# Optimization experiments

Measured on AMD Instinct MI355X. Metric: run time of the kernel, lower is better.

Reference implementation:

```python
import jax, jax.numpy as jnp
import numpy as np

MAX_DIST = 10
N_OUT = 8


def setup_inputs() -> dict:
    key = jax.random.key(0)
    k1, k2 = jax.random.split(key)
    B, N = 32, 512
    adjacency = jax.random.uniform(k1, (B, N, N), dtype=jnp.float32)
    node_mask = jnp.ones((B, N), dtype=bool)
    # learned embedding table: (max_distance + 2, n_out)
    emb = jax.random.normal(k2, (MAX_DIST + 2, N_OUT), dtype=jnp.float32)
    return {"adjacency": adjacency, "node_mask": node_mask, "emb": emb}


def reference(adjacency, node_mask, emb):
    # BFS distances computed under no_grad in the original -> stop_gradient
    adjacency = jax.lax.stop_gradient(adjacency)
    B, N, _ = adjacency.shape
    adj_bin = adjacency > 0.5
    adj_sym = adj_bin | jnp.swapaxes(adj_bin, -1, -2)
    pair_valid = node_mask[:, :, None] & node_mask[:, None, :]  # (B,N,N)
    adj_sym = adj_sym & pair_valid
    adj_f = adj_sym.astype(jnp.float32)

    UNREACH = MAX_DIST + 1
    eye = jnp.eye(N, dtype=bool)[None]                 # (1,N,N)
    dist = jnp.where(eye, 0, UNREACH).astype(jnp.int32)  # broadcasts to (B,N,N) later
    reach = jnp.broadcast_to(eye, (B, N, N))

    # iterative BFS: reach_{k+1} = (reach_k @ adj > 0) | reach_k
    for k in range(1, MAX_DIST + 1):
        reach_next = (jnp.einsum('bij,bjk->bik', reach.astype(jnp.float32), adj_f) > 0) | reach
        frontier = reach_next & ~reach
        dist = jnp.where(frontier, jnp.int32(k), dist)
        reach = reach_next

    dist = jnp.where(pair_valid, dist, UNREACH)  # invalid pairs -> UNREACHABLE
    return emb[dist]  # (B,N,N,n_out)
```

## Files before the change

### kernel.cpp

```cpp
#include <hip/hip_runtime.h>
#include <stdint.h>

typedef unsigned long long u64;
typedef float vf4 __attribute__((ext_vector_type(4)));

#define NB 32
#define N 512
#define MAXD 10
#define NW 8
#define ST 516
#define PB 8

__global__ __launch_bounds__(256) void k1_pack(const float* __restrict__ adj,
                                               const int* __restrict__ mask,
                                               u64* __restrict__ gsym) {
    __shared__ float ldsA[64 * 65];
    __shared__ float ldsB[64 * 65];
    __shared__ unsigned char mI[64], mJ[64];
    int p = blockIdx.x;
    int b = blockIdx.y;
    int ti = 0;
    while (p >= 8 - ti) { p -= 8 - ti; ++ti; }
    int tj = ti + p;
    int i0 = ti * 64, j0 = tj * 64;
    int t = threadIdx.x;
    if (t < 64) mI[t] = (mask[b * N + i0 + t] != 0);
    else if (t < 128) mJ[t - 64] = (mask[b * N + j0 + (t - 64)] != 0);
    const float* Ab = adj + (size_t)b * N * N;
    #pragma unroll
    for (int s = 0; s < 4; ++s) {
        int idx = t + 256 * s;
        int r = idx >> 4, c4 = idx & 15;
        float4 va = *(const float4*)&Ab[(size_t)(i0 + r) * N + j0 + c4 * 4];
        float4 vb = *(const float4*)&Ab[(size_t)(j0 + r) * N + i0 + c4 * 4];
        int o = r * 65 + c4 * 4;
        ldsA[o] = va.x; ldsA[o + 1] = va.y; ldsA[o + 2] = va.z; ldsA[o + 3] = va.w;
        ldsB[o] = vb.x; ldsB[o + 1] = vb.y; ldsB[o + 2] = vb.z; ldsB[o + 3] = vb.w;
    }
    __syncthreads();
    int wave = t >> 6, lane = t & 63;
    for (int s = 0; s < 16; ++s) {
        int r = wave * 16 + s;
        bool bit = ((ldsA[r * 65 + lane] > 0.5f) || (ldsB[lane * 65 + r] > 0.5f))
                   && mI[r] && mJ[lane];
        u64 word = __ballot(bit);
        if (lane == 0) gsym[((size_t)b * N + i0 + r) * NW + tj] = word;
    }
    for (int s = 0; s < 16; ++s) {
        int r = wave * 16 + s;
        bool bit = ((ldsB[r * 65 + lane] > 0.5f) || (ldsA[lane * 65 + r] > 0.5f))
                   && mJ[r] && mI[lane];
        u64 word = __ballot(bit);
        if (lane == 0) gsym[((size_t)b * N + j0 + r) * NW + ti] = word;
    }
}

__device__ __forceinline__ u64 spread8(unsigned b) {
    u64 x = (u64)(b * 0x01010101u);
    x |= x << 32;
    x &= 0x8040201008040201ULL;
    x += 0x7f7f7f7f7f7f7f7fULL;
    return (x >> 7) & 0x0101010101010101ULL;
}

__global__ __launch_bounds__(256) void k2_bfs(const u64* __restrict__ gsym,
                                              const int* __restrict__ mask,
                                              u64* __restrict__ distw) {
    __shared__ u64 adjT[NW * ST];
    __shared__ u64 outB[64 * 65];
    int blk = blockIdx.x;
    int b = blk >> 3;
    int r0 = (blk & 7) * 64;
    int t = threadIdx.x;
    const u64* gs = gsym + (size_t)b * N * NW;
    for (int q = t; q < N * NW; q += 256) {
        u64 w = gs[q];
        adjT[(q & 7) * ST + (q >> 3)] = w;
    }
    __syncthreads();

    if (t < 64) {
        int i = r0 + t;
        bool mi = mask[b * N + i] != 0;
        u64 c0[NW], c1[NW], c2[NW], c3[NW];
        #pragma unroll
        for (int w = 0; w < NW; ++w) { c0[w] = 0; c1[w] = 0; c2[w] = 0; c3[w] = 0; }

        if (mi) {
            u64 reach[NW] = {};
            u64 frontier[NW] = {};
            reach[i >> 6] = 1ULL << (i & 63);
            #pragma unroll
            for (int w = 0; w < NW; ++w) frontier[w] = reach[w];
            bool active = true;
            for (int k = 0; k <= MAXD; ++k) {
                u64 nr_any = 0;
                #pragma unroll
                for (int w = 0; w < NW; ++w) {
                    u64 u = ~reach[w];
                    nr_any |= u;
                    u64 t0 = c0[w] & u; c0[w] ^= u;
                    u64 t1 = c1[w] & t0; c1[w] ^= t0;
                    u64 t2 = c2[w] & t1; c2[w] ^= t1;
                    c3[w] ^= t2;
                }
                if (nr_any == 0) break;
                if (k == MAXD) break;
                if (active) {
                    u64 acc[NW] = {};
                    bool sat = false;
                    for (int w = 0; w < NW && !sat; ++w) {
                        u64 f = frontier[w];
                        while (f && !sat) {
                            int jlast = w << 6;
                            #pragma unroll
                            for (int u = 0; u < PB; ++u) {
                                int j = f ? ((w << 6) + __builtin_ctzll(f)) : jlast;
                                jlast = j;
                                f &= f - 1;
                                #pragma unroll
                                for (int e = 0; e < NW; ++e) acc[e] |= adjT[e * ST + j];
                            }
                            u64 all = acc[0];
                            #pragma unroll
                            for (int e = 1; e < NW; ++e) all &= acc[e];
                            sat = (all == ~0ULL);
                        }
                    }
                    bool any = false;
                    #pragma unroll
                    for (int w = 0; w < NW; ++w) {
                        u64 nf = acc[w] & ~reach[w];
                        frontier[w] = nf;
                        reach[w] |= nf;
                        any = any || (nf != 0);
                    }
                    active = any;
                }
            }
        } else {
            #pragma unroll
            for (int w = 0; w < NW; ++w) { c0[w] = ~0ULL; c1[w] = ~0ULL; c3[w] = ~0ULL; }
        }

        #pragma unroll
        for (int w = 0; w < NW; ++w) {
            #pragma unroll
            for (int h = 0; h < 8; ++h) {
                unsigned b0 = (unsigned)(c0[w] >> (8 * h)) & 0xFF;
                unsigned b1 = (unsigned)(c1[w] >> (8 * h)) & 0xFF;
                unsigned b2 = (unsigned)(c2[w] >> (8 * h)) & 0xFF;
                unsigned b3 = (unsigned)(c3[w] >> (8 * h)) & 0xFF;
                outB[t * 65 + w * 8 + h] =
                    spread8(b0) | (spread8(b1) << 1) | (spread8(b2) << 2) | (spread8(b3) << 3);
            }
        }
    }
    __syncthreads();

    u64* dp = distw + ((size_t)(b * N + r0)) * 64;
    for (int q = t; q < 64 * 64; q += 256) {
        dp[q] = outB[(q >> 6) * 65 + (q & 63)];
    }
}

__global__ __launch_bounds__(256) void k3_expand(const u64* __restrict__ distw,
                                                 const float* __restrict__ emb,
                                                 vf4* __restrict__ out4) {
    __shared__ vf4 e4[(MAXD + 2) * 2];
    int t = threadIdx.x;
    if (t < (MAXD + 2) * 2) e4[t] = ((const vf4*)emb)[t];
    __syncthreads();
    const unsigned char* __restrict__ db = (const unsigned char*)distw;
    size_t dbase = (size_t)blockIdx.x * 4096;
    const unsigned char* dp = db + dbase;
    vf4* op = out4 + dbase * 2;
    int h = t & 1;
    int tb = t >> 1;
    #pragma unroll 8
    for (int g = 0; g < 16; ++g) {
        int d0 = dp[g * 256 + tb];
        int d1 = dp[g * 256 + 128 + tb];
        vf4 v0 = e4[d0 * 2 + h];
        vf4 v1 = e4[d1 * 2 + h];
        op[g * 512 + t] = v0;
        op[g * 512 + 256 + t] = v1;
    }
}

extern "C" void kernel_launch(void* const* d_in, const int* in_sizes, int n_in,
                              void* d_out, int out_size, void* d_ws, size_t ws_size,
                              hipStream_t stream) {
    const float* adj = (const float*)d_in[0];
    const int* mask = (const int*)d_in[1];
    const float* emb = (const float*)d_in[2];
    u64* distw = (u64*)d_ws;
    u64* gsym = (u64*)((char*)d_ws + (size_t)NB * N * N);
    k1_pack<<<dim3(36, NB), 256, 0, stream>>>(adj, mask, gsym);
    k2_bfs<<<dim3(NB * 8), 256, 0, stream>>>(gsym, mask, distw);
    k3_expand<<<dim3(2048), 256, 0, stream>>>(distw, emb, (vf4*)d_out);
}
```

Measured before the change: 326.4 us.

## Pack adjacency tiles via direct ballots and bit-matrix shuffle transpose

Rewrites the packing kernel so each wave reads rows of both tiles straight from global memory and ballots them into 64-bit words, removing the float LDS staging tiles. The symmetric OR is then formed by transposing the 64x64 bit matrix in registers with a six-stage butterfly of cross-lane shuffles, and masks are applied as ballot words. This cuts LDS traffic and shared memory use in the pack step. In exchange the global loads become scalar-per-lane instead of float4, and only two waves do the transpose and store.

```diff
diff --git a/kernel.cpp b/kernel.cpp
--- a/kernel.cpp
+++ b/kernel.cpp
@@ -14,44 +14,52 @@
 __global__ __launch_bounds__(256) void k1_pack(const float* __restrict__ adj,
                                                const int* __restrict__ mask,
                                                u64* __restrict__ gsym) {
-    __shared__ float ldsA[64 * 65];
-    __shared__ float ldsB[64 * 65];
-    __shared__ unsigned char mI[64], mJ[64];
+    __shared__ u64 pa[64];
+    __shared__ u64 pb[64];
+    __shared__ u64 mwIJ[2];
     int p = blockIdx.x;
     int b = blockIdx.y;
     int ti = 0;
     while (p >= 8 - ti) { p -= 8 - ti; ++ti; }
     int tj = ti + p;
     int i0 = ti * 64, j0 = tj * 64;
-    int t = threadIdx.x;
-    if (t < 64) mI[t] = (mask[b * N + i0 + t] != 0);
-    else if (t < 128) mJ[t - 64] = (mask[b * N + j0 + (t - 64)] != 0);
+    int t = threadIdx.x, wave = t >> 6, lane = t & 63;
     const float* Ab = adj + (size_t)b * N * N;
-    #pragma unroll
-    for (int s = 0; s < 4; ++s) {
-        int idx = t + 256 * s;
-        int r = idx >> 4, c4 = idx & 15;
-        float4 va = *(const float4*)&Ab[(size_t)(i0 + r) * N + j0 + c4 * 4];
-        float4 vb = *(const float4*)&Ab[(size_t)(j0 + r) * N + i0 + c4 * 4];
-        int o = r * 65 + c4 * 4;
-        ldsA[o] = va.x; ldsA[o + 1] = va.y; ldsA[o + 2] = va.z; ldsA[o + 3] = va.w;
-        ldsB[o] = vb.x; ldsB[o + 1] = vb.y; ldsB[o + 2] = vb.z; ldsB[o + 3] = vb.w;
-    }
-    __syncthreads();
-    int wave = t >> 6, lane = t & 63;
+    #pragma unroll 4
     for (int s = 0; s < 16; ++s) {
         int r = wave * 16 + s;
-        bool bit = ((ldsA[r * 65 + lane] > 0.5f) || (ldsB[lane * 65 + r] > 0.5f))
-                   && mI[r] && mJ[lane];
-        u64 word = __ballot(bit);
-        if (lane == 0) gsym[((size_t)b * N + i0 + r) * NW + tj] = word;
-    }
-    for (int s = 0; s < 16; ++s) {
-        int r = wave * 16 + s;
-        bool bit = ((ldsB[r * 65 + lane] > 0.5f) || (ldsA[lane * 65 + r] > 0.5f))
-                   && mJ[r] && mI[lane];
-        u64 word = __ballot(bit);
-        if (lane == 0) gsym[((size_t)b * N + j0 + r) * NW + ti] = word;
+        bool ba = Ab[(size_t)(i0 + r) * N + j0 + lane] > 0.5f;
+        u64 wa = __ballot(ba);
+        bool bb = Ab[(size_t)(j0 + r) * N + i0 + lane] > 0.5f;
+        u64 wb = __ballot(bb);
+        if (lane == 0) { pa[r] = wa; pb[r] = wb; }
+    }
+    if (wave < 2) {
+        u64 m = __ballot(mask[b * N + (wave == 0 ? i0 : j0) + lane] != 0);
+        if (lane == 0) mwIJ[wave] = m;
+    }
+    __syncthreads();
+
+    if (wave < 2) {
+        u64 x = (wave == 0) ? pb[lane] : pa[lane];
+        const u64 Hm[6] = {0xFFFFFFFF00000000ULL, 0xFFFF0000FFFF0000ULL,
+                           0xFF00FF00FF00FF00ULL, 0xF0F0F0F0F0F0F0F0ULL,
+                           0xCCCCCCCCCCCCCCCCULL, 0xAAAAAAAAAAAAAAAAULL};
+        #pragma unroll
+        for (int k = 0; k < 6; ++k) {
+            int j = 32 >> k;
+            u64 H = Hm[k];
+            u64 y = (u64)__shfl_xor((unsigned long long)x, j);
+            x = ((lane & j) == 0) ? ((x & ~H) | ((y << j) & H))
+                                  : ((x & H) | ((y >> j) & ~H));
+        }
+        u64 own  = (wave == 0) ? pa[lane] : pb[lane];
+        u64 mrow = mwIJ[wave];
+        u64 mcol = mwIJ[wave ^ 1];
+        u64 outw = (own | x) & (((mrow >> lane) & 1) ? mcol : 0ULL);
+        size_t row = (size_t)b * N + (wave == 0 ? i0 : j0) + lane;
+        int wt = (wave == 0) ? tj : ti;
+        gsym[row * NW + wt] = outw;
     }
 }
 
```

New measurement: 318.1 us, median of 2. 2.5% less time.
